# Optimization experiments

Hardware: AMD Instinct MI355X
Metric: run time of the kernel (lower is better)

Reference implementation:

```python
import jax, jax.numpy as jnp
import numpy as np

EPS = 1e-12  # matches torch F.normalize clamp_min eps


def agnn_conv(x, src, dst, beta, num_nodes):
    # x: [N, H]; src/dst: [E'] (self-loops already included)
    norm = jnp.sqrt(jnp.sum(x * x, axis=-1, keepdims=True))
    x_norm = x / jnp.maximum(norm, EPS)
    # edge-wise cosine similarity scaled by beta
    logits = beta * jnp.sum(x_norm[src] * x_norm[dst], axis=-1)  # [E']
    # scatter-softmax over incoming edges of each destination node
    m = jax.ops.segment_max(logits, dst, num_segments=num_nodes)  # [N]
    e = jnp.exp(logits - m[dst])
    s = jax.ops.segment_sum(e, dst, num_segments=num_nodes)       # [N]
    alpha = e / s[dst]                                            # [E']
    # weighted scatter-add aggregation of source features
    return jax.ops.segment_sum(alpha[:, None] * x[src], dst, num_segments=num_nodes)


def setup_inputs() -> dict:
    key = jax.random.key(0)
    ks = jax.random.split(key, 8)
    N, E, C_in, C_hid, C_out = 100000, 1600000, 512, 128, 64
    x = jax.random.normal(ks[0], (N, C_in), dtype=jnp.float32)
    edge_index = jax.random.randint(ks[1], (2, E), 0, N, dtype=jnp.int64)
    W1 = jax.random.normal(ks[2], (C_in, C_hid), dtype=jnp.float32) / np.sqrt(C_in)
    b1 = jnp.zeros((C_hid,), dtype=jnp.float32)
    W2 = jax.random.normal(ks[3], (C_hid, C_out), dtype=jnp.float32) / np.sqrt(C_hid)
    b2 = jnp.zeros((C_out,), dtype=jnp.float32)
    beta2 = jnp.array(1.0, dtype=jnp.float32)  # learned beta of prop2; prop1 beta fixed at 1.0
    return {"x": x, "edge_index": edge_index, "W1": W1, "b1": b1,
            "beta2": beta2, "W2": W2, "b2": b2}


def reference(x, edge_index, W1, b1, beta2, W2, b2):
    N = x.shape[0]
    # AGNNConv adds self-loops by default
    loops = jnp.arange(N, dtype=edge_index.dtype)
    src = jnp.concatenate([edge_index[0], loops])
    dst = jnp.concatenate([edge_index[1], loops])
    # dropout is identity in eval mode
    h = jax.nn.relu(x @ W1 + b1)                      # [N, hidden]
    h = agnn_conv(h, src, dst, jnp.float32(1.0), N)   # prop1 (beta frozen = 1)
    h = agnn_conv(h, src, dst, beta2, N)              # prop2 (learned beta)
    logits = h @ W2 + b2                              # [N, out]
    return jax.nn.log_softmax(logits, axis=1)
```

## Files before the change

kernel.cpp:

```cpp
#include <hip/hip_runtime.h>
#include <math.h>


static inline int divup(int a, int b) { return (a + b - 1) / b; }

typedef __attribute__((ext_vector_type(8))) short short8;
typedef __attribute__((ext_vector_type(4))) float f32x4;
union U16 { uint4 u; short8 s; };

__device__ __forceinline__ unsigned bf16r(float f) {
    unsigned u = __float_as_uint(f);
    return (u + 0x7FFFu + ((u >> 16) & 1u)) >> 16;
}
__device__ __forceinline__ unsigned pack2(float a, float b) {
    return bf16r(a) | (bf16r(b) << 16);
}
__device__ __forceinline__ float bflo(unsigned u) { return __uint_as_float(u << 16); }
__device__ __forceinline__ float bfhi(unsigned u) { return __uint_as_float(u & 0xFFFF0000u); }

__global__ __launch_bounds__(64) void k_detect(const int* __restrict__ raw, int* flag) {
    int t = threadIdx.x;
    int v = raw[2 * t + 1];
    unsigned long long b = __ballot(v != 0);
    if (t == 0) *flag = (b == 0ULL) ? 1 : 0;
}

__global__ __launch_bounds__(256) void k_cvt(const int* __restrict__ raw, int E,
                                             const int* __restrict__ flag,
                                             int* __restrict__ s32, int* __restrict__ d32,
                                             int* __restrict__ cnt) {
    int i = blockIdx.x * blockDim.x + threadIdx.x;
    if (i >= E) return;
    int s, d;
    if (*flag) {
        s = raw[2 * (size_t)i];
        d = raw[2 * ((size_t)E + i)];
    } else {
        s = raw[i];
        d = raw[(size_t)E + i];
    }
    s32[i] = s;
    d32[i] = d;
    atomicAdd(&cnt[d], 1);
}

__global__ __launch_bounds__(1024) void k_scan1(const int* __restrict__ cnt, int N,
                                                int* __restrict__ rp, int* __restrict__ bsum) {
    __shared__ int sm[1024];
    int t = threadIdx.x;
    int i = blockIdx.x * 1024 + t;
    int v = (i < N) ? cnt[i] + 1 : 0;
    sm[t] = v;
    __syncthreads();
#pragma unroll
    for (int off = 1; off < 1024; off <<= 1) {
        int u = (t >= off) ? sm[t - off] : 0;
        __syncthreads();
        sm[t] += u;
        __syncthreads();
    }
    if (i < N) rp[i] = sm[t] - v;
    if (t == 1023) bsum[blockIdx.x] = sm[t];
}

__global__ __launch_bounds__(64) void k_scan2(int* __restrict__ bsum, int nb) {
    if (threadIdx.x == 0) {
        int run = 0;
        for (int i = 0; i < nb; ++i) { int v = bsum[i]; bsum[i] = run; run += v; }
    }
}

__global__ __launch_bounds__(256) void k_scan3(int* __restrict__ rp, const int* __restrict__ bsum,
                                               int N, int Etot, int* __restrict__ cursor) {
    int i = blockIdx.x * blockDim.x + threadIdx.x;
    if (i < N) {
        int v = rp[i] + bsum[i >> 10];
        rp[i] = v;
        cursor[i] = v;
    } else if (i == N) {
        rp[N] = Etot;
    }
}

__global__ __launch_bounds__(256) void k_scatter(const int* __restrict__ s32,
                                                 const int* __restrict__ d32, int E, int N,
                                                 int* __restrict__ cursor,
                                                 int* __restrict__ esrc) {
    int b = blockIdx.x;
    int xcd = b & 7;
    int nstripe = gridDim.x >> 3;
    int stripe = b >> 3;
    int lo = (int)(((long long)xcd * N) >> 3);
    int hi = (int)(((long long)(xcd + 1) * N) >> 3);
    int Etot = E + N;
    for (int e = stripe * 256 + threadIdx.x; e < Etot; e += nstripe * 256) {
        int d = (e < E) ? d32[e] : (e - E);
        if (d < lo || d >= hi) continue;
        int s = (e < E) ? s32[e] : d;
        int pos = atomicAdd(&cursor[d], 1);
        esrc[pos] = s;
    }
}

__global__ __launch_bounds__(256) void k_cvtW1(const float* __restrict__ W1,
                                               unsigned short* __restrict__ W1t) {
    int i = blockIdx.x * 256 + threadIdx.x;
    if (i >= 512 * 128) return;
    int k = i >> 7, n = i & 127;
    W1t[n * 512 + k] = (unsigned short)bf16r(W1[i]);
}

__global__ __launch_bounds__(256) void k_cvtW2(const float* __restrict__ W2,
                                               unsigned short* __restrict__ W2t) {
    int i = blockIdx.x * 256 + threadIdx.x;
    if (i >= 128 * 64) return;
    int k = i >> 6, n = i & 63;
    W2t[n * 128 + k] = (unsigned short)bf16r(W2[i]);
}

#define XSW(c, off) ((off) ^ (((c) & 7) << 4))
__global__ __launch_bounds__(256) void k_gemm1(const float* __restrict__ x,
                                               const unsigned short* __restrict__ W1t,
                                               const float* __restrict__ b1, int N,
                                               unsigned short* __restrict__ xh1,
                                               float* __restrict__ n1) {
    __shared__ __align__(16) unsigned char lds[65536];
    const int tid = threadIdx.x;
    const int lane = tid & 63;
    const int lt = lane & 15, lg = lane >> 4;
    const int w = tid >> 6;
    const int row0 = blockIdx.x * 128;

    const float* xb[2];
#pragma unroll
    for (int rf = 0; rf < 2; ++rf) {
        int r = row0 + w * 32 + rf * 16 + lt;
        if (r > N - 1) r = N - 1;
        xb[rf] = x + (size_t)r * 512 + lg * 8;
    }

    f32x4 acc[2][8];
#pragma unroll
    for (int i = 0; i < 2; ++i)
#pragma unroll
        for (int j = 0; j < 8; ++j) acc[i][j] = (f32x4){0.f, 0.f, 0.f, 0.f};

    for (int ph = 0; ph < 2; ++ph) {
        const int kb = ph * 256;
        float4 ac[2][2], an[2][2];
#pragma unroll
        for (int rf = 0; rf < 2; ++rf) {
            ac[rf][0] = ((const float4*)(xb[rf] + kb))[0];
            ac[rf][1] = ((const float4*)(xb[rf] + kb))[1];
        }
        __syncthreads();
        {
            int c = tid >> 1, h = tid & 1;
            const uint4* wp = (const uint4*)(W1t + c * 512 + kb + h * 128);
            unsigned char* base = lds + c * 512;
#pragma unroll
            for (int i = 0; i < 16; ++i)
                *(uint4*)(base + XSW(c, h * 256 + i * 16)) = wp[i];
        }
        __syncthreads();

#pragma unroll
        for (int ks = 0; ks < 8; ++ks) {
            if (ks < 7) {
#pragma unroll
                for (int rf = 0; rf < 2; ++rf) {
                    an[rf][0] = ((const float4*)(xb[rf] + kb + (ks + 1) * 32))[0];
                    an[rf][1] = ((const float4*)(xb[rf] + kb + (ks + 1) * 32))[1];
                }
            }
            U16 af[2];
#pragma unroll
            for (int rf = 0; rf < 2; ++rf) {
                af[rf].u.x = pack2(ac[rf][0].x, ac[rf][0].y);
                af[rf].u.y = pack2(ac[rf][0].z, ac[rf][0].w);
                af[rf].u.z = pack2(ac[rf][1].x, ac[rf][1].y);
                af[rf].u.w = pack2(ac[rf][1].z, ac[rf][1].w);
            }
#pragma unroll
            for (int cf = 0; cf < 8; ++cf) {
                int col = cf * 16 + lt;
                U16 bf;
                bf.u = *(const uint4*)(lds + col * 512 + XSW(col, ks * 64 + lg * 16));
#pragma unroll
                for (int rf = 0; rf < 2; ++rf)
                    acc[rf][cf] = __builtin_amdgcn_mfma_f32_16x16x32_bf16(
                        af[rf].s, bf.s, acc[rf][cf], 0, 0, 0);
            }
            if (ks < 7) {
#pragma unroll
                for (int rf = 0; rf < 2; ++rf) {
                    ac[rf][0] = an[rf][0];
                    ac[rf][1] = an[rf][1];
                }
            }
        }
    }

    float bias[8];
#pragma unroll
    for (int cf = 0; cf < 8; ++cf) bias[cf] = b1[cf * 16 + lt];
    float* sc = (float*)lds;
    unsigned char* pk = lds + 36864;
#pragma unroll 1
    for (int p = 0; p < 2; ++p) {
        __syncthreads();
        if ((w >> 1) == p) {
#pragma unroll
            for (int rf = 0; rf < 2; ++rf)
#pragma unroll
                for (int reg = 0; reg < 4; ++reg) {
                    int rl = (w & 1) * 32 + rf * 16 + lg * 4 + reg;
#pragma unroll
                    for (int cf = 0; cf < 8; ++cf)
                        sc[rl * 132 + cf * 16 + lt] =
                            fmaxf(acc[rf][cf][reg] + bias[cf], 0.f);
                }
        }
        __syncthreads();
        {
            int rl = tid >> 2, q = tid & 3;
            int gr = row0 + p * 64 + rl;
            const float* rowp = sc + rl * 132 + q * 32;
            float v[32];
#pragma unroll
            for (int i = 0; i < 8; ++i) {
                float4 f = ((const float4*)rowp)[i];
                v[4 * i] = f.x; v[4 * i + 1] = f.y; v[4 * i + 2] = f.z; v[4 * i + 3] = f.w;
            }
            float s2 = 0.f;
#pragma unroll
            for (int i = 0; i < 32; ++i) s2 += v[i] * v[i];
            s2 += __shfl_xor(s2, 1, 64);
            s2 += __shfl_xor(s2, 2, 64);
            float nrm = sqrtf(s2);
            float rn = 1.0f / fmaxf(nrm, 1e-12f);
            uint4 o[4];
            unsigned* op = (unsigned*)o;
#pragma unroll
            for (int i = 0; i < 16; ++i)
                op[i] = pack2(v[2 * i] * rn, v[2 * i + 1] * rn);
            uint4* pd = (uint4*)(pk + rl * 256 + q * 64);
            pd[0] = o[0]; pd[1] = o[1]; pd[2] = o[2]; pd[3] = o[3];
            if (q == 0 && gr < N) n1[gr] = nrm;
        }
        __syncthreads();
#pragma unroll
        for (int j = 0; j < 4; ++j) {
            int boff = j * 4096 + tid * 16;
            int r = boff >> 8;
            int gr = row0 + p * 64 + r;
            if (gr < N)
                *(uint4*)((unsigned char*)xh1 + (size_t)gr * 256 + (boff & 255)) =
                    *(const uint4*)(pk + boff);
        }
    }
}

__global__ __launch_bounds__(256) void k_conv(const unsigned short* __restrict__ xh,
                                              const float* __restrict__ nrmt,
                                              const int* __restrict__ rp,
                                              const int* __restrict__ esrc, int N,
                                              const float* __restrict__ betap,
                                              unsigned short* __restrict__ outh,
                                              float* __restrict__ outn) {
    int node = (blockIdx.x * blockDim.x + threadIdx.x) >> 6;
    if (node >= N) return;
    int lane = threadIdx.x & 63;
    int t = lane & 15, g = lane >> 4;
    float beta = betap ? *betap : 1.0f;

    uint4 hdu = *(const uint4*)&xh[(size_t)node * 128 + 8 * t];
    float hd[8];
    hd[0] = bflo(hdu.x); hd[1] = bfhi(hdu.x);
    hd[2] = bflo(hdu.y); hd[3] = bfhi(hdu.y);
    hd[4] = bflo(hdu.z); hd[5] = bfhi(hdu.z);
    hd[6] = bflo(hdu.w); hd[7] = bfhi(hdu.w);

    int e0 = rp[node], e1 = rp[node + 1];
    float acc[8] = {0.f, 0.f, 0.f, 0.f, 0.f, 0.f, 0.f, 0.f};
    float ssum = 0.f;

    for (int cs = e0; cs < e1; cs += 64) {
        int el = cs + lane;
        int sidx = esrc[(el < e1) ? el : e0];
        float nsl = nrmt[sidx];
        int R = e1 - cs;
        if (R > 64) R = 64;
        int nr = (R + 3) >> 2;

        int sA = __shfl(sidx, g, 64);
        float nsA = __shfl(nsl, g, 64);
        uint4 rowA = *(const uint4*)&xh[(size_t)sA * 128 + 8 * t];

        for (int r = 0; r < nr; ++r) {
            const bool hasNext = (r + 1) < nr;
            uint4 rowB;
            float nsB = 0.f;
            if (hasNext) {
                int sB = __shfl(sidx, 4 * (r + 1) + g, 64);
                nsB = __shfl(nsl, 4 * (r + 1) + g, 64);
                rowB = *(const uint4*)&xh[(size_t)sB * 128 + 8 * t];
            }
            float v[8];
            v[0] = bflo(rowA.x); v[1] = bfhi(rowA.x);
            v[2] = bflo(rowA.y); v[3] = bfhi(rowA.y);
            v[4] = bflo(rowA.z); v[5] = bfhi(rowA.z);
            v[6] = bflo(rowA.w); v[7] = bfhi(rowA.w);
            float p = 0.f;
#pragma unroll
            for (int j = 0; j < 8; ++j) p += v[j] * hd[j];
            p += __shfl_xor(p, 1, 64);
            p += __shfl_xor(p, 2, 64);
            p += __shfl_xor(p, 4, 64);
            p += __shfl_xor(p, 8, 64);
            int e = cs + 4 * r + g;
            float w = (e < e1) ? __expf(p * beta) : 0.f;
            float wn = w * nsA;
            ssum += w;
#pragma unroll
            for (int j = 0; j < 8; ++j) acc[j] += wn * v[j];
            if (hasNext) {
                rowA = rowB;
                nsA = nsB;
            }
        }
    }
#pragma unroll
    for (int j = 0; j < 8; ++j) {
        acc[j] += __shfl_xor(acc[j], 16, 64);
        acc[j] += __shfl_xor(acc[j], 32, 64);
    }
    ssum += __shfl_xor(ssum, 16, 64);
    ssum += __shfl_xor(ssum, 32, 64);
    float r = 1.0f / ssum;

    if (outn == nullptr) {
        if (g == 0) {
            uint4 q;
            q.x = pack2(acc[0] * r, acc[1] * r);
            q.y = pack2(acc[2] * r, acc[3] * r);
            q.z = pack2(acc[4] * r, acc[5] * r);
            q.w = pack2(acc[6] * r, acc[7] * r);
            *(uint4*)&outh[(size_t)node * 128 + 8 * t] = q;
        }
    } else {
        float o[8];
        float s2 = 0.f;
#pragma unroll
        for (int j = 0; j < 8; ++j) { o[j] = acc[j] * r; s2 += o[j] * o[j]; }
        s2 += __shfl_xor(s2, 1, 64);
        s2 += __shfl_xor(s2, 2, 64);
        s2 += __shfl_xor(s2, 4, 64);
        s2 += __shfl_xor(s2, 8, 64);
        float nn = sqrtf(s2);
        float rn = 1.0f / fmaxf(nn, 1e-12f);
        if (g == 0) {
            uint4 q;
            q.x = pack2(o[0] * rn, o[1] * rn);
            q.y = pack2(o[2] * rn, o[3] * rn);
            q.z = pack2(o[4] * rn, o[5] * rn);
            q.w = pack2(o[6] * rn, o[7] * rn);
            *(uint4*)&outh[(size_t)node * 128 + 8 * t] = q;
            if (t == 0) outn[node] = nn;
        }
    }
}

#define G2_ASTRIDE 272
__global__ __launch_bounds__(256) void k_gemm2(const unsigned short* __restrict__ h,
                                               const unsigned short* __restrict__ W2t,
                                               const float* __restrict__ b2, int N,
                                               float* __restrict__ out) {
    __shared__ __align__(16) unsigned char As[128 * G2_ASTRIDE];
    __shared__ __align__(16) unsigned char Bs[64 * G2_ASTRIDE];
    const int tid = threadIdx.x;
    const int lane = tid & 63;
    const int lt = lane & 15, lg = lane >> 4;
    const int wid = tid >> 6;
    const int row0 = blockIdx.x * 128;

    {
        int arow = tid >> 1, ahalf = tid & 1;
        const uint4* src = (const uint4*)(h + (size_t)(row0 + arow) * 128 + ahalf * 64);
        unsigned char* ab = As + arow * G2_ASTRIDE + ahalf * 128;
#pragma unroll
        for (int i = 0; i < 8; ++i) ((uint4*)ab)[i] = src[i];
        int brow = tid >> 2, bq = tid & 3;
        const uint4* bs = (const uint4*)(W2t + (size_t)brow * 128 + bq * 32);
        unsigned char* bb = Bs + brow * G2_ASTRIDE + bq * 64;
#pragma unroll
        for (int i = 0; i < 4; ++i) ((uint4*)bb)[i] = bs[i];
    }
    __syncthreads();

    f32x4 acc[2][4];
#pragma unroll
    for (int i = 0; i < 2; ++i)
#pragma unroll
        for (int j = 0; j < 4; ++j) acc[i][j] = (f32x4){0.f, 0.f, 0.f, 0.f};

#pragma unroll
    for (int sub = 0; sub < 4; ++sub) {
        U16 af[2], bf[4];
#pragma unroll
        for (int mi = 0; mi < 2; ++mi)
            af[mi].u = *(const uint4*)(As + (wid * 32 + mi * 16 + lt) * G2_ASTRIDE + sub * 64 + lg * 16);
#pragma unroll
        for (int ni = 0; ni < 4; ++ni)
            bf[ni].u = *(const uint4*)(Bs + (ni * 16 + lt) * G2_ASTRIDE + sub * 64 + lg * 16);
#pragma unroll
        for (int mi = 0; mi < 2; ++mi)
#pragma unroll
            for (int ni = 0; ni < 4; ++ni)
                acc[mi][ni] = __builtin_amdgcn_mfma_f32_16x16x32_bf16(
                    af[mi].s, bf[ni].s, acc[mi][ni], 0, 0, 0);
    }

    float bias[4];
#pragma unroll
    for (int ni = 0; ni < 4; ++ni) bias[ni] = b2[ni * 16 + lt];

#pragma unroll
    for (int mi = 0; mi < 2; ++mi) {
#pragma unroll
        for (int reg = 0; reg < 4; ++reg) {
            int row = row0 + wid * 32 + mi * 16 + lg * 4 + reg;
            if (row < N) {
                float v[4];
#pragma unroll
                for (int ni = 0; ni < 4; ++ni) v[ni] = acc[mi][ni][reg] + bias[ni];
                float m = fmaxf(fmaxf(v[0], v[1]), fmaxf(v[2], v[3]));
                m = fmaxf(m, __shfl_xor(m, 1, 64));
                m = fmaxf(m, __shfl_xor(m, 2, 64));
                m = fmaxf(m, __shfl_xor(m, 4, 64));
                m = fmaxf(m, __shfl_xor(m, 8, 64));
                float s = __expf(v[0] - m) + __expf(v[1] - m) +
                          __expf(v[2] - m) + __expf(v[3] - m);
                s += __shfl_xor(s, 1, 64);
                s += __shfl_xor(s, 2, 64);
                s += __shfl_xor(s, 4, 64);
                s += __shfl_xor(s, 8, 64);
                float lg2 = logf(s);
#pragma unroll
                for (int ni = 0; ni < 4; ++ni)
                    out[(size_t)row * 64 + ni * 16 + lt] = v[ni] - m - lg2;
            }
        }
    }
}

extern "C" void kernel_launch(void* const* d_in, const int* in_sizes, int n_in,
                              void* d_out, int out_size, void* d_ws, size_t ws_size,
                              hipStream_t stream) {
    const float* x     = (const float*)d_in[0];
    const int*   ei    = (const int*)d_in[1];
    const float* W1    = (const float*)d_in[2];
    const float* b1    = (const float*)d_in[3];
    const float* beta2 = (const float*)d_in[4];
    const float* W2    = (const float*)d_in[5];
    const float* b2    = (const float*)d_in[6];
    float* out = (float*)d_out;

    const int N = in_sizes[0] / 512;
    const int E = in_sizes[1] / 2;
    const int Etot = E + N;

    char* ws = (char*)d_ws;
    size_t off = 0;
    auto alloc = [&](size_t bytes) -> void* {
        void* p = ws + off;
        off = (off + bytes + 511) & ~(size_t)511;
        return p;
    };
    unsigned short* t1 = (unsigned short*)alloc((size_t)N * 128 * 2);
    unsigned short* t2 = (unsigned short*)alloc((size_t)N * 128 * 2);
    float* n1   = (float*)alloc((size_t)N * 4);
    float* n2   = (float*)alloc((size_t)N * 4);
    int* cnt    = (int*)alloc((size_t)N * 4);
    int* rp     = (int*)alloc((size_t)(N + 1) * 4);
    int* cursor = (int*)alloc((size_t)N * 4);
    int* bsum   = (int*)alloc(4096);
    int* flag   = (int*)alloc(512);
    unsigned short* W1t = (unsigned short*)alloc(512 * 128 * 2);
    unsigned short* W2t = (unsigned short*)alloc(128 * 64 * 2);
    int* s32    = (int*)alloc((size_t)E * 4);
    int* d32    = (int*)alloc((size_t)E * 4);
    int* esrc   = (int*)alloc((size_t)Etot * 4);
    (void)ws_size; (void)n_in; (void)out_size;

    (void)hipMemsetAsync(cnt, 0, (size_t)N * 4, stream);

    k_detect<<<1, 64, 0, stream>>>(ei, flag);
    k_cvt<<<divup(E, 256), 256, 0, stream>>>(ei, E, flag, s32, d32, cnt);
    int nb = divup(N, 1024);
    k_scan1<<<nb, 1024, 0, stream>>>(cnt, N, rp, bsum);
    k_scan2<<<1, 64, 0, stream>>>(bsum, nb);
    k_scan3<<<divup(N + 1, 256), 256, 0, stream>>>(rp, bsum, N, Etot, cursor);
    k_scatter<<<2048, 256, 0, stream>>>(s32, d32, E, N, cursor, esrc);

    k_cvtW1<<<divup(512 * 128, 256), 256, 0, stream>>>(W1, W1t);
    k_cvtW2<<<divup(128 * 64, 256), 256, 0, stream>>>(W2, W2t);

    k_gemm1<<<divup(N, 128), 256, 0, stream>>>(x, W1t, b1, N, t1, n1);
    k_conv<<<divup(N, 4), 256, 0, stream>>>(t1, n1, rp, esrc, N, nullptr, t2, n2);
    k_conv<<<divup(N, 4), 256, 0, stream>>>(t2, n2, rp, esrc, N, beta2, t1, nullptr);
    k_gemm2<<<divup(N, 128), 256, 0, stream>>>(t1, W2t, b2, N, out);
}
```

Measured before the change: 405.1 us.

## Shrink gemm1 tile to 64 rows with 32KB LDS and 4 K-phases

Halves the row tile of the first GEMM from 128 to 64 rows per block, so each wave handles one 16-row fragment instead of two. The W1 staging is split into four 128-wide K phases, which cuts LDS from 64KB to 32KB, and the A-operand prefetch now runs across phase boundaries. The epilogue is reworked for 32-row passes with padded row strides. The aim is more blocks per CU and more blocks overall for this memory-bound GEMM over x. The cost is that W1 is reloaded from global memory twice as often in total, and there are more barriers per block.

```diff
diff --git a/kernel.cpp b/kernel.cpp
--- a/kernel.cpp
+++ b/kernel.cpp
@@ -124,79 +124,61 @@
                                                const float* __restrict__ b1, int N,
                                                unsigned short* __restrict__ xh1,
                                                float* __restrict__ n1) {
-    __shared__ __align__(16) unsigned char lds[65536];
+    __shared__ __align__(16) unsigned char lds[32768];
     const int tid = threadIdx.x;
     const int lane = tid & 63;
     const int lt = lane & 15, lg = lane >> 4;
     const int w = tid >> 6;
-    const int row0 = blockIdx.x * 128;
-
-    const float* xb[2];
-#pragma unroll
-    for (int rf = 0; rf < 2; ++rf) {
-        int r = row0 + w * 32 + rf * 16 + lt;
-        if (r > N - 1) r = N - 1;
-        xb[rf] = x + (size_t)r * 512 + lg * 8;
-    }
-
-    f32x4 acc[2][8];
-#pragma unroll
-    for (int i = 0; i < 2; ++i)
-#pragma unroll
-        for (int j = 0; j < 8; ++j) acc[i][j] = (f32x4){0.f, 0.f, 0.f, 0.f};
-
-    for (int ph = 0; ph < 2; ++ph) {
-        const int kb = ph * 256;
-        float4 ac[2][2], an[2][2];
-#pragma unroll
-        for (int rf = 0; rf < 2; ++rf) {
-            ac[rf][0] = ((const float4*)(xb[rf] + kb))[0];
-            ac[rf][1] = ((const float4*)(xb[rf] + kb))[1];
-        }
+    const int row0 = blockIdx.x * 64;
+
+    int arow = row0 + w * 16 + lt;
+    if (arow > N - 1) arow = N - 1;
+    const float* xb = x + (size_t)arow * 512 + lg * 8;
+
+    f32x4 acc[8];
+#pragma unroll
+    for (int j = 0; j < 8; ++j) acc[j] = (f32x4){0.f, 0.f, 0.f, 0.f};
+
+    float4 ac[2], an[2];
+    ac[0] = ((const float4*)xb)[0];
+    ac[1] = ((const float4*)xb)[1];
+
+    for (int ph = 0; ph < 4; ++ph) {
+        const int kb = ph * 128;
         __syncthreads();
         {
             int c = tid >> 1, h = tid & 1;
-            const uint4* wp = (const uint4*)(W1t + c * 512 + kb + h * 128);
-            unsigned char* base = lds + c * 512;
-#pragma unroll
-            for (int i = 0; i < 16; ++i)
-                *(uint4*)(base + XSW(c, h * 256 + i * 16)) = wp[i];
-        }
-        __syncthreads();
-
-#pragma unroll
-        for (int ks = 0; ks < 8; ++ks) {
-            if (ks < 7) {
-#pragma unroll
-                for (int rf = 0; rf < 2; ++rf) {
-                    an[rf][0] = ((const float4*)(xb[rf] + kb + (ks + 1) * 32))[0];
-                    an[rf][1] = ((const float4*)(xb[rf] + kb + (ks + 1) * 32))[1];
-                }
-            }
-            U16 af[2];
-#pragma unroll
-            for (int rf = 0; rf < 2; ++rf) {
-                af[rf].u.x = pack2(ac[rf][0].x, ac[rf][0].y);
-                af[rf].u.y = pack2(ac[rf][0].z, ac[rf][0].w);
-                af[rf].u.z = pack2(ac[rf][1].x, ac[rf][1].y);
-                af[rf].u.w = pack2(ac[rf][1].z, ac[rf][1].w);
-            }
+            const uint4* wp = (const uint4*)(W1t + c * 512 + kb + h * 64);
+            unsigned char* base = lds + c * 256;
+#pragma unroll
+            for (int i = 0; i < 8; ++i)
+                *(uint4*)(base + XSW(c, h * 128 + i * 16)) = wp[i];
+        }
+        __syncthreads();
+
+#pragma unroll
+        for (int ks = 0; ks < 4; ++ks) {
+            const int kg = ph * 4 + ks;
+            if (kg < 15) {
+                an[0] = ((const float4*)(xb + (kg + 1) * 32))[0];
+                an[1] = ((const float4*)(xb + (kg + 1) * 32))[1];
+            }
+            U16 af;
+            af.u.x = pack2(ac[0].x, ac[0].y);
+            af.u.y = pack2(ac[0].z, ac[0].w);
+            af.u.z = pack2(ac[1].x, ac[1].y);
+            af.u.w = pack2(ac[1].z, ac[1].w);
 #pragma unroll
             for (int cf = 0; cf < 8; ++cf) {
                 int col = cf * 16 + lt;
                 U16 bf;
-                bf.u = *(const uint4*)(lds + col * 512 + XSW(col, ks * 64 + lg * 16));
-#pragma unroll
-                for (int rf = 0; rf < 2; ++rf)
-                    acc[rf][cf] = __builtin_amdgcn_mfma_f32_16x16x32_bf16(
-                        af[rf].s, bf.s, acc[rf][cf], 0, 0, 0);
-            }
-            if (ks < 7) {
-#pragma unroll
-                for (int rf = 0; rf < 2; ++rf) {
-                    ac[rf][0] = an[rf][0];
-                    ac[rf][1] = an[rf][1];
-                }
+                bf.u = *(const uint4*)(lds + col * 256 + XSW(col, ks * 64 + lg * 16));
+                acc[cf] = __builtin_amdgcn_mfma_f32_16x16x32_bf16(
+                    af.s, bf.s, acc[cf], 0, 0, 0);
+            }
+            if (kg < 15) {
+                ac[0] = an[0];
+                ac[1] = an[1];
             }
         }
     }
@@ -205,58 +187,59 @@
 #pragma unroll
     for (int cf = 0; cf < 8; ++cf) bias[cf] = b1[cf * 16 + lt];
     float* sc = (float*)lds;
-    unsigned char* pk = lds + 36864;
+    unsigned char* pk = lds + 16896;
 #pragma unroll 1
     for (int p = 0; p < 2; ++p) {
         __syncthreads();
         if ((w >> 1) == p) {
 #pragma unroll
-            for (int rf = 0; rf < 2; ++rf)
-#pragma unroll
-                for (int reg = 0; reg < 4; ++reg) {
-                    int rl = (w & 1) * 32 + rf * 16 + lg * 4 + reg;
-#pragma unroll
-                    for (int cf = 0; cf < 8; ++cf)
-                        sc[rl * 132 + cf * 16 + lt] =
-                            fmaxf(acc[rf][cf][reg] + bias[cf], 0.f);
-                }
+            for (int reg = 0; reg < 4; ++reg) {
+                int rl = (w & 1) * 16 + lg * 4 + reg;
+#pragma unroll
+                for (int cf = 0; cf < 8; ++cf)
+                    sc[rl * 132 + cf * 16 + lt] =
+                        fmaxf(acc[cf][reg] + bias[cf], 0.f);
+            }
         }
         __syncthreads();
         {
-            int rl = tid >> 2, q = tid & 3;
-            int gr = row0 + p * 64 + rl;
-            const float* rowp = sc + rl * 132 + q * 32;
-            float v[32];
-#pragma unroll
-            for (int i = 0; i < 8; ++i) {
+            int rl = tid >> 3, q = tid & 7;
+            int gr = row0 + p * 32 + rl;
+            const float* rowp = sc + rl * 132 + q * 16;
+            float v[16];
+#pragma unroll
+            for (int i = 0; i < 4; ++i) {
                 float4 f = ((const float4*)rowp)[i];
                 v[4 * i] = f.x; v[4 * i + 1] = f.y; v[4 * i + 2] = f.z; v[4 * i + 3] = f.w;
             }
             float s2 = 0.f;
 #pragma unroll
-            for (int i = 0; i < 32; ++i) s2 += v[i] * v[i];
+            for (int i = 0; i < 16; ++i) s2 += v[i] * v[i];
             s2 += __shfl_xor(s2, 1, 64);
             s2 += __shfl_xor(s2, 2, 64);
+            s2 += __shfl_xor(s2, 4, 64);
             float nrm = sqrtf(s2);
             float rn = 1.0f / fmaxf(nrm, 1e-12f);
-            uint4 o[4];
+            uint4 o[2];
             unsigned* op = (unsigned*)o;
 #pragma unroll
-            for (int i = 0; i < 16; ++i)
+            for (int i = 0; i < 8; ++i)
                 op[i] = pack2(v[2 * i] * rn, v[2 * i + 1] * rn);
-            uint4* pd = (uint4*)(pk + rl * 256 + q * 64);
-            pd[0] = o[0]; pd[1] = o[1]; pd[2] = o[2]; pd[3] = o[3];
+            uint4* pd = (uint4*)(pk + rl * 272 + q * 32);
+            pd[0] = o[0];
+            pd[1] = o[1];
             if (q == 0 && gr < N) n1[gr] = nrm;
         }
         __syncthreads();
 #pragma unroll
-        for (int j = 0; j < 4; ++j) {
+        for (int j = 0; j < 2; ++j) {
             int boff = j * 4096 + tid * 16;
             int r = boff >> 8;
-            int gr = row0 + p * 64 + r;
+            int inner = boff & 255;
+            int gr = row0 + p * 32 + r;
             if (gr < N)
-                *(uint4*)((unsigned char*)xh1 + (size_t)gr * 256 + (boff & 255)) =
-                    *(const uint4*)(pk + boff);
+                *(uint4*)((unsigned char*)xh1 + (size_t)gr * 256 + inner) =
+                    *(const uint4*)(pk + r * 272 + inner);
         }
     }
 }
@@ -506,7 +489,7 @@
     k_cvtW1<<<divup(512 * 128, 256), 256, 0, stream>>>(W1, W1t);
     k_cvtW2<<<divup(128 * 64, 256), 256, 0, stream>>>(W2, W2t);
 
-    k_gemm1<<<divup(N, 128), 256, 0, stream>>>(x, W1t, b1, N, t1, n1);
+    k_gemm1<<<divup(N, 64), 256, 0, stream>>>(x, W1t, b1, N, t1, n1);
     k_conv<<<divup(N, 4), 256, 0, stream>>>(t1, n1, rp, esrc, N, nullptr, t2, n2);
     k_conv<<<divup(N, 4), 256, 0, stream>>>(t2, n2, rp, esrc, N, beta2, t1, nullptr);
     k_gemm2<<<divup(N, 128), 256, 0, stream>>>(t1, W2t, b2, N, out);
```

Result: faster. 395.3 us (-2.4%).
